# Kernel optimization log

Measured on AMD Instinct MI355X. Metric: run time of the kernel, lower is better.

The kernel has to match this reference:

```python
import jax, jax.numpy as jnp
import numpy as np

E = 256   # embed_dim
H = 8     # num_heads
D = E // H  # head_dim = 32
L = 1024  # seq len (Q_len == K_len == V_len)


def setup_inputs() -> dict:
    key = jax.random.key(0)
    ks = jax.random.split(key, 10)
    f = lambda k, s: jax.random.normal(k, s, dtype=jnp.float32)
    return {
        "V": f(ks[0], (L, E)),
        "K": f(ks[1], (L, E)),
        "Q": f(ks[2], (L, E)),
        # genomic-style coordinates, strictly positive
        "position": jax.random.uniform(ks[3], (L,), dtype=jnp.float32) * 1e5,
        "Wq": f(ks[4], (E, E)) * 0.02,
        "Wk": f(ks[5], (E, E)) * 0.02,
        "Wv": f(ks[6], (E, E)) * 0.02,
        "Wr": f(ks[7], (E, 1)) * 0.02,   # K_relative_linear weight [out=E, in=1]
        "Wo": f(ks[8], (E, E)) * 0.02,
        "bo": jnp.zeros((E,), jnp.float32),
    }


def reference(V, K, Q, position, Wq, Wk, Wv, Wr, Wo, bo):
    Lq = Q.shape[0]
    # projections (nn.Linear: x @ W.T), split into heads -> (L, H, D)
    q = (Q @ Wq.T).reshape(Lq, H, D)
    k = (K @ Wk.T).reshape(Lq, H, D)
    v = (V @ Wv.T).reshape(Lq, H, D)

    # relative position scalar per (q, k) pair: log(|p_q - p_k| + 1)
    rel = jnp.log(jnp.abs(position[:, None] - position[None, :]) + 1.0)  # (L, L)

    # K_relative_linear maps scalar rel -> (H, D); the einsum
    # 'nqhd,nhqjd->nhqj' then factorizes exactly as:
    #   sum_d Q[q,h,d] * rel[q,j] * Wr[h,d] = (Q . Wr)[h,q] * rel[q,j]
    # so we avoid materializing the (H, L, L, D) tensor while computing
    # mathematically identical results.
    Wr_h = Wr[:, 0].reshape(H, D)                    # (H, D)
    coeff = jnp.einsum('qhd,hd->hq', q, Wr_h)        # (H, L)

    energy = jnp.einsum('qhd,khd->hqk', q, k)        # (H, L, L)
    energy = energy + coeff[:, :, None] * rel[None, :, :]

    attn = jax.nn.softmax(energy / np.float32(E) ** 0.5, axis=2)
    out = jnp.einsum('hqk,khd->qhd', attn, v).reshape(Lq, E)
    out = out @ Wo.T + bo
    return out
```

## Files before the change

### kernel.cpp

```cpp
#include <hip/hip_runtime.h>
#include <math.h>

#define EDIM 256
#define LDIM 1024
#define HDIM 8
#define DDIM 32

typedef __attribute__((ext_vector_type(8))) short short8;
typedef __attribute__((ext_vector_type(4))) float f32x4;
typedef __attribute__((ext_vector_type(4))) unsigned u32x4;

__device__ inline unsigned short bf16h(float x) {
    unsigned u = __float_as_uint(x);
    return (unsigned short)((u + 0x7fff + ((u >> 16) & 1)) >> 16);
}
__device__ inline float bf16tof(unsigned short h) {
    return __uint_as_float(((unsigned)h) << 16);
}
__device__ inline unsigned packsplit(float x) {
    unsigned u = __float_as_uint(x);
    float r = x - __uint_as_float(u & 0xffff0000u);
    return (u & 0xffff0000u) | (unsigned)bf16h(r);
}
__device__ inline unsigned packsplit_rne(float x) {
    unsigned short h = bf16h(x);
    float r = x - bf16tof(h);
    return ((unsigned)h << 16) | (unsigned)bf16h(r);
}

__global__ __launch_bounds__(256) void proj_kernel(
    const float* __restrict__ Q, const float* __restrict__ Km, const float* __restrict__ V,
    const float* __restrict__ Wq, const float* __restrict__ Wk, const float* __restrict__ Wv,
    const float* __restrict__ Wr,
    unsigned* __restrict__ qT, unsigned* __restrict__ kT, unsigned* __restrict__ vT,
    float* __restrict__ coeff)
{
    const int z = blockIdx.z;
    const float* __restrict__ X = (z == 0) ? Q : (z == 1) ? Km : V;
    const float* __restrict__ W = (z == 0) ? Wq : (z == 1) ? Wk : Wv;
    unsigned* __restrict__ dst  = (z == 0) ? qT : (z == 1) ? kT : vT;

    const int n0 = blockIdx.x * 32;
    const int o0 = blockIdx.y * 32;
    const int tid = threadIdx.x;
    const int wave = tid >> 6, lane = tid & 63;
    const int n = lane & 15, quad = lane >> 4;
    const int rh = wave & 1, oh = wave >> 1;

    const int s    = tid >> 7;
    const int r    = (tid >> 2) & 31;
    const int qd   = tid & 3;
    const int half = r >> 4;
    const int fl8  = ((r & 15) | (qd << 4)) * 8;

    __shared__ short Xhi[2][2][512], Xlo[2][2][512];
    __shared__ short Whi[2][2][512], Wlo[2][2][512];
    __shared__ float cpart[2][2][16];

    const float* xp = X + (n0 + r) * EDIM + s * 32 + qd * 8;
    const float* wp = W + (o0 + r) * EDIM + s * 32 + qd * 8;

    float4 xa0 = *(const float4*)xp, xa1 = *(const float4*)(xp + 4);
    float4 wa0 = *(const float4*)wp, wa1 = *(const float4*)(wp + 4);

    f32x4 acc = {0.f, 0.f, 0.f, 0.f};

    for (int kb = 0; kb < EDIM; kb += 64) {
        __syncthreads();
        {
            float xv[8] = {xa0.x,xa0.y,xa0.z,xa0.w, xa1.x,xa1.y,xa1.z,xa1.w};
            float wv[8] = {wa0.x,wa0.y,wa0.z,wa0.w, wa1.x,wa1.y,wa1.z,wa1.w};
            short8 xh, xl, wh, wl;
            #pragma unroll
            for (int j = 0; j < 8; ++j) {
                unsigned px = packsplit_rne(xv[j]);
                unsigned pw = packsplit_rne(wv[j]);
                xh[j] = (short)(px >> 16); xl[j] = (short)(px & 0xffffu);
                wh[j] = (short)(pw >> 16); wl[j] = (short)(pw & 0xffffu);
            }
            *(short8*)&Xhi[s][half][fl8] = xh;
            *(short8*)&Xlo[s][half][fl8] = xl;
            *(short8*)&Whi[s][half][fl8] = wh;
            *(short8*)&Wlo[s][half][fl8] = wl;
        }
        float4 xn0, xn1, wn0, wn1;
        if (kb + 64 < EDIM) {
            xn0 = *(const float4*)(xp + kb + 64); xn1 = *(const float4*)(xp + kb + 68);
            wn0 = *(const float4*)(wp + kb + 64); wn1 = *(const float4*)(wp + kb + 68);
        }
        __syncthreads();
        #pragma unroll
        for (int ss = 0; ss < 2; ++ss) {
            short8 ah = *(const short8*)&Xhi[ss][rh][lane*8];
            short8 al = *(const short8*)&Xlo[ss][rh][lane*8];
            short8 bh = *(const short8*)&Whi[ss][oh][lane*8];
            short8 bl = *(const short8*)&Wlo[ss][oh][lane*8];
            acc = __builtin_amdgcn_mfma_f32_16x16x32_bf16(al, bh, acc, 0, 0, 0);
            acc = __builtin_amdgcn_mfma_f32_16x16x32_bf16(ah, bl, acc, 0, 0, 0);
            acc = __builtin_amdgcn_mfma_f32_16x16x32_bf16(ah, bh, acc, 0, 0, 0);
        }
        xa0 = xn0; xa1 = xn1; wa0 = wn0; wa1 = wn1;
    }

    const int h  = o0 >> 5;
    const int og = oh * 16 + n;
    #pragma unroll
    for (int i = 0; i < 4; ++i) {
        const int row = rh * 16 + 4 * quad + i;
        dst[(h * LDIM + n0 + row) * DDIM + og] = packsplit_rne(acc[i]);
    }

    if (z == 0) {
        const float wr = Wr[o0 + og];
        #pragma unroll
        for (int i = 0; i < 4; ++i) {
            float c = acc[i] * wr;
            c += __shfl_xor(c, 1, 64);
            c += __shfl_xor(c, 2, 64);
            c += __shfl_xor(c, 4, 64);
            c += __shfl_xor(c, 8, 64);
            if (n == 0) cpart[rh][oh][4*quad + i] = c;
        }
        __syncthreads();
        if (tid < 32)
            coeff[h * LDIM + n0 + tid] = cpart[tid >> 4][0][tid & 15]
                                       + cpart[tid >> 4][1][tid & 15];
    }
}

__global__ __launch_bounds__(256, 4) void attn_kernel(
    const unsigned* __restrict__ qT, const unsigned* __restrict__ kT, const unsigned* __restrict__ vT,
    const float* __restrict__ coeff, const float* __restrict__ pos,
    float* __restrict__ Op, float* __restrict__ Mp, float* __restrict__ Lp, int nkt)
{
    const int h   = blockIdx.y;
    const int q0  = blockIdx.x * 64;
    const int p   = blockIdx.z;
    const int kt0 = p * nkt * 64;
    const int tid  = threadIdx.x;
    const int wave = tid >> 6;
    const int lane = tid & 63;
    const int n    = lane & 15;
    const int quad = lane >> 4;
    const int qs0  = wave * 16;

    __shared__ __align__(16) short khi[4*64*8];
    __shared__ __align__(16) short klo[4*64*8];
    __shared__ __align__(16) unsigned vs2[32][68];
    __shared__ __align__(16) unsigned pA[64][68];
    __shared__ float pk[64];

    short8 qhi, qlo;
    {
        const unsigned* qp = qT + (h*LDIM + q0 + qs0 + n) * DDIM + quad*8;
        u32x4 a0 = *(const u32x4*)qp;
        u32x4 a1 = *(const u32x4*)(qp + 4);
        #pragma unroll
        for (int j = 0; j < 4; ++j) {
            qhi[j]   = (short)(a0[j] >> 16);  qlo[j]   = (short)(a0[j] & 0xffffu);
            qhi[j+4] = (short)(a1[j] >> 16);  qlo[j+4] = (short)(a1[j] & 0xffffu);
        }
    }

    float pq[4], cq[4];
    #pragma unroll
    for (int i = 0; i < 4; ++i) {
        const int r = q0 + qs0 + 4*quad + i;
        pq[i] = pos[r];
        cq[i] = coeff[h*LDIM + r] * 0.0625f;
    }

    float m[4], l[4];
    #pragma unroll
    for (int i = 0; i < 4; ++i) { m[i] = -INFINITY; l[i] = 0.f; }

    f32x4 of0 = {0.f,0.f,0.f,0.f}, of1 = {0.f,0.f,0.f,0.f};

    const int cS = tid >> 2;
    const int dq = tid & 3;
    const int lane2 = (cS & 15) | (dq << 4);
    const int gS = cS >> 4;

    u32x4 k0c, k1c, v0c, v1c; float pkc = 0.f;
    {
        const unsigned* kp = kT + (h*LDIM + kt0 + cS) * DDIM + dq*8;
        k0c = *(const u32x4*)kp; k1c = *(const u32x4*)(kp + 4);
        const unsigned* vp = vT + (h*LDIM + kt0 + cS) * DDIM + dq*8;
        v0c = *(const u32x4*)vp; v1c = *(const u32x4*)(vp + 4);
        if (tid < 64) pkc = pos[kt0 + tid];
    }

    for (int t = 0; t < nkt; ++t) {
        __syncthreads();

        {
            short8 hi8, lo8;
            #pragma unroll
            for (int j = 0; j < 4; ++j) {
                hi8[j]   = (short)(k0c[j] >> 16);  lo8[j]   = (short)(k0c[j] & 0xffffu);
                hi8[j+4] = (short)(k1c[j] >> 16);  lo8[j+4] = (short)(k1c[j] & 0xffffu);
            }
            *((short8*)&khi[(gS*64 + lane2)*8]) = hi8;
            *((short8*)&klo[(gS*64 + lane2)*8]) = lo8;
            #pragma unroll
            for (int j = 0; j < 4; ++j) {
                vs2[dq*8 + j][cS]     = v0c[j];
                vs2[dq*8 + j + 4][cS] = v1c[j];
            }
            if (tid < 64) pk[tid] = pkc;
        }

        u32x4 k0n, k1n, v0n, v1n; float pkn = 0.f;
        if (t + 1 < nkt) {
            const int kt = kt0 + (t+1) * 64;
            const unsigned* kp = kT + (h*LDIM + kt + cS) * DDIM + dq*8;
            k0n = *(const u32x4*)kp; k1n = *(const u32x4*)(kp + 4);
            const unsigned* vp = vT + (h*LDIM + kt + cS) * DDIM + dq*8;
            v0n = *(const u32x4*)vp; v1n = *(const u32x4*)(vp + 4);
            if (tid < 64) pkn = pos[kt + tid];
        }
        __syncthreads();

        f32x4 Sf[4];
        #pragma unroll
        for (int t4 = 0; t4 < 4; ++t4) {
            short8 bhi = *((const short8*)&khi[(t4*64 + lane)*8]);
            short8 blo = *((const short8*)&klo[(t4*64 + lane)*8]);
            f32x4 acc = {0.f, 0.f, 0.f, 0.f};
            acc = __builtin_amdgcn_mfma_f32_16x16x32_bf16(qlo, bhi, acc, 0, 0, 0);
            acc = __builtin_amdgcn_mfma_f32_16x16x32_bf16(qhi, blo, acc, 0, 0, 0);
            acc = __builtin_amdgcn_mfma_f32_16x16x32_bf16(qhi, bhi, acc, 0, 0, 0);
            Sf[t4] = acc;
        }

        float ev[4][4];
        float rmax[4] = {-INFINITY, -INFINITY, -INFINITY, -INFINITY};
        #pragma unroll
        for (int t4 = 0; t4 < 4; ++t4) {
            const float pkt = pk[16*t4 + n];
            #pragma unroll
            for (int i = 0; i < 4; ++i) {
                float s = fmaf(Sf[t4][i], 0.0625f, cq[i] * __logf(fabsf(pq[i] - pkt) + 1.f));
                ev[t4][i] = s;
                rmax[i] = fmaxf(rmax[i], s);
            }
        }
        #pragma unroll
        for (int off = 1; off < 16; off <<= 1)
            #pragma unroll
            for (int i = 0; i < 4; ++i)
                rmax[i] = fmaxf(rmax[i], __shfl_xor(rmax[i], off, 64));

        float al[4], rsum[4];
        #pragma unroll
        for (int i = 0; i < 4; ++i) {
            const float mn = fmaxf(m[i], rmax[i]);
            al[i] = __expf(m[i] - mn);
            m[i] = mn;
            rsum[i] = 0.f;
        }
        #pragma unroll
        for (int t4 = 0; t4 < 4; ++t4)
            #pragma unroll
            for (int i = 0; i < 4; ++i) {
                float e = __expf(ev[t4][i] - m[i]);
                rsum[i] += e;
                pA[qs0 + 4*quad + i][16*t4 + n] = packsplit(e);
            }
        #pragma unroll
        for (int off = 1; off < 16; off <<= 1)
            #pragma unroll
            for (int i = 0; i < 4; ++i)
                rsum[i] += __shfl_xor(rsum[i], off, 64);
        #pragma unroll
        for (int i = 0; i < 4; ++i) l[i] = l[i]*al[i] + rsum[i];

        #pragma unroll
        for (int i = 0; i < 4; ++i) { of0[i] *= al[i]; of1[i] *= al[i]; }

        #pragma unroll
        for (int ch = 0; ch < 2; ++ch) {
            const unsigned* ap = &pA[qs0 + n][ch*32 + quad*8];
            u32x4 a0 = *(const u32x4*)ap;
            u32x4 a1 = *(const u32x4*)(ap + 4);
            short8 phi, plo;
            #pragma unroll
            for (int j = 0; j < 4; ++j) {
                phi[j]   = (short)(a0[j] >> 16);
                plo[j]   = (short)(a0[j] & 0xffffu);
                phi[j+4] = (short)(a1[j] >> 16);
                plo[j+4] = (short)(a1[j] & 0xffffu);
            }
            #pragma unroll
            for (int dt = 0; dt < 2; ++dt) {
                const unsigned* vp = &vs2[dt*16 + n][ch*32 + quad*8];
                u32x4 b0 = *(const u32x4*)vp;
                u32x4 b1 = *(const u32x4*)(vp + 4);
                short8 vhi, vlo;
                #pragma unroll
                for (int j = 0; j < 4; ++j) {
                    vhi[j]   = (short)(b0[j] >> 16);
                    vlo[j]   = (short)(b0[j] & 0xffffu);
                    vhi[j+4] = (short)(b1[j] >> 16);
                    vlo[j+4] = (short)(b1[j] & 0xffffu);
                }
                f32x4& of = dt ? of1 : of0;
                of = __builtin_amdgcn_mfma_f32_16x16x32_bf16(plo, vhi, of, 0, 0, 0);
                of = __builtin_amdgcn_mfma_f32_16x16x32_bf16(phi, vlo, of, 0, 0, 0);
                of = __builtin_amdgcn_mfma_f32_16x16x32_bf16(phi, vhi, of, 0, 0, 0);
            }
        }

        k0c = k0n; k1c = k1n; v0c = v0n; v1c = v1n; pkc = pkn;
    }

    const int ph = p * HDIM + h;
    {
        const size_t base = ((size_t)ph * LDIM + q0 + qs0) * DDIM;
        #pragma unroll
        for (int i = 0; i < 4; ++i) {
            Op[base + (size_t)(4*quad + i)*DDIM + n]      = of0[i];
            Op[base + (size_t)(4*quad + i)*DDIM + 16 + n] = of1[i];
        }
    }
    if (n == 0) {
        #pragma unroll
        for (int i = 0; i < 4; ++i) {
            const int r = q0 + qs0 + 4*quad + i;
            Mp[ph*LDIM + r] = m[i];
            Lp[ph*LDIM + r] = l[i];
        }
    }
}

__global__ __launch_bounds__(256) void combine_kernel(
    const float* __restrict__ Op, const float* __restrict__ Mp, const float* __restrict__ Lp,
    int P, float* __restrict__ A)
{
    const int idx = blockIdx.x * 256 + threadIdx.x;
    const int n  = idx >> 6;
    const int e4 = (idx & 63) * 4;
    const int h  = e4 >> 5;
    const int d  = e4 & 31;

    float mv[8], lv[8];
    float mx = -INFINITY;
    #pragma unroll
    for (int p = 0; p < 8; ++p) if (p < P) {
        mv[p] = Mp[(p*HDIM + h)*LDIM + n];
        lv[p] = Lp[(p*HDIM + h)*LDIM + n];
        mx = fmaxf(mx, mv[p]);
    }
    float s = 0.f;
    #pragma unroll
    for (int p = 0; p < 8; ++p) if (p < P) {
        float a = __expf(mv[p] - mx);
        mv[p] = a;
        s += a * lv[p];
    }
    const float inv = 1.f / s;

    float4 x; x.x = x.y = x.z = x.w = 0.f;
    #pragma unroll
    for (int p = 0; p < 8; ++p) if (p < P) {
        const float sp = mv[p] * inv;
        float4 xp = *(const float4*)(Op + ((size_t)(p*HDIM + h)*LDIM + n)*DDIM + d);
        x.x += sp*xp.x; x.y += sp*xp.y; x.z += sp*xp.z; x.w += sp*xp.w;
    }
    *(float4*)(A + n*EDIM + e4) = x;
}

__global__ __launch_bounds__(256) void outproj_kernel(
    const float* __restrict__ A, const float* __restrict__ Wo,
    const float* __restrict__ bo, float* __restrict__ out)
{
    const int n0 = blockIdx.x * 32;
    const int o0 = blockIdx.y * 32;
    const int tid = threadIdx.x;
    const int wave = tid >> 6, lane = tid & 63;
    const int n = lane & 15, quad = lane >> 4;
    const int rh = wave & 1, oh = wave >> 1;

    const int s    = tid >> 7;
    const int r    = (tid >> 2) & 31;
    const int qd   = tid & 3;
    const int half = r >> 4;
    const int fl8  = ((r & 15) | (qd << 4)) * 8;

    __shared__ short Xhi[2][2][512], Xlo[2][2][512];
    __shared__ short Whi[2][2][512], Wlo[2][2][512];

    const float* xp = A  + (n0 + r) * EDIM + s * 32 + qd * 8;
    const float* wp = Wo + (o0 + r) * EDIM + s * 32 + qd * 8;

    float4 xa0 = *(const float4*)xp, xa1 = *(const float4*)(xp + 4);
    float4 wa0 = *(const float4*)wp, wa1 = *(const float4*)(wp + 4);

    f32x4 acc = {0.f, 0.f, 0.f, 0.f};

    for (int kb = 0; kb < EDIM; kb += 64) {
        __syncthreads();
        {
            float xv[8] = {xa0.x,xa0.y,xa0.z,xa0.w, xa1.x,xa1.y,xa1.z,xa1.w};
            float wv[8] = {wa0.x,wa0.y,wa0.z,wa0.w, wa1.x,wa1.y,wa1.z,wa1.w};
            short8 xh, xl, wh, wl;
            #pragma unroll
            for (int j = 0; j < 8; ++j) {
                unsigned px = packsplit_rne(xv[j]);
                unsigned pw = packsplit_rne(wv[j]);
                xh[j] = (short)(px >> 16); xl[j] = (short)(px & 0xffffu);
                wh[j] = (short)(pw >> 16); wl[j] = (short)(pw & 0xffffu);
            }
            *(short8*)&Xhi[s][half][fl8] = xh;
            *(short8*)&Xlo[s][half][fl8] = xl;
            *(short8*)&Whi[s][half][fl8] = wh;
            *(short8*)&Wlo[s][half][fl8] = wl;
        }
        float4 xn0, xn1, wn0, wn1;
        if (kb + 64 < EDIM) {
            xn0 = *(const float4*)(xp + kb + 64); xn1 = *(const float4*)(xp + kb + 68);
            wn0 = *(const float4*)(wp + kb + 64); wn1 = *(const float4*)(wp + kb + 68);
        }
        __syncthreads();
        #pragma unroll
        for (int ss = 0; ss < 2; ++ss) {
            short8 ah = *(const short8*)&Xhi[ss][rh][lane*8];
            short8 al = *(const short8*)&Xlo[ss][rh][lane*8];
            short8 bh = *(const short8*)&Whi[ss][oh][lane*8];
            short8 bl = *(const short8*)&Wlo[ss][oh][lane*8];
            acc = __builtin_amdgcn_mfma_f32_16x16x32_bf16(al, bh, acc, 0, 0, 0);
            acc = __builtin_amdgcn_mfma_f32_16x16x32_bf16(ah, bl, acc, 0, 0, 0);
            acc = __builtin_amdgcn_mfma_f32_16x16x32_bf16(ah, bh, acc, 0, 0, 0);
        }
        xa0 = xn0; xa1 = xn1; wa0 = wn0; wa1 = wn1;
    }

    const int og = o0 + oh*16 + n;
    const float b = bo[og];
    #pragma unroll
    for (int i = 0; i < 4; ++i) {
        const int row = n0 + rh*16 + 4*quad + i;
        out[row * EDIM + og] = acc[i] + b;
    }
}

extern "C" void kernel_launch(void* const* d_in, const int* in_sizes, int n_in,
                              void* d_out, int out_size, void* d_ws, size_t ws_size,
                              hipStream_t stream) {
    const float* V   = (const float*)d_in[0];
    const float* K   = (const float*)d_in[1];
    const float* Q   = (const float*)d_in[2];
    const float* pos = (const float*)d_in[3];
    const float* Wq  = (const float*)d_in[4];
    const float* Wk  = (const float*)d_in[5];
    const float* Wv  = (const float*)d_in[6];
    const float* Wr  = (const float*)d_in[7];
    const float* Wo  = (const float*)d_in[8];
    const float* bo  = (const float*)d_in[9];
    float* out = (float*)d_out;
    float* ws  = (float*)d_ws;

    auto need = [](int P) -> size_t {
        return (size_t)(794624 + P*278528) * 4;
    };
    int P = 2;
    if (ws_size >= need(8)) P = 8;
    else if (ws_size >= need(4)) P = 4;

    unsigned* qT = (unsigned*)ws;
    unsigned* kT = (unsigned*)(ws + 262144);
    unsigned* vT = (unsigned*)(ws + 524288);
    float* coeff = ws + 786432;
    float* Op    = ws + 794624;
    float* Mp    = Op + (size_t)P * 262144;
    float* Lp    = Mp + (size_t)P * 8192;
    float* A     = ws;

    proj_kernel   <<<dim3(32, 8, 3), 256, 0, stream>>>(Q, K, V, Wq, Wk, Wv, Wr, qT, kT, vT, coeff);
    attn_kernel   <<<dim3(16, 8, P), 256, 0, stream>>>(qT, kT, vT, coeff, pos, Op, Mp, Lp, 16 / P);
    combine_kernel<<<dim3(256),      256, 0, stream>>>(Op, Mp, Lp, P, A);
    outproj_kernel<<<dim3(32, 8),    256, 0, stream>>>(A, Wo, bo, out);
}
```

Baseline: 106.8 us.

## Store bf16 hi/lo planes separately, fuse combine with out-projection, use exp2/log2

Projection outputs are now written as separate bf16 hi and lo arrays, so the attention kernel loads MFMA operands directly without unpacking. The same planar layout is used for the P tile and the V tile in shared memory. Exp and log switch to the hardware exp2/log2 instructions, with the softmax scale folded into a log2e-adjusted constant. The combine and output-projection kernels are merged into one kernel that reads a pre-split Wo produced by an extra z-slice of the projection launch, removing one launch and the intermediate A buffer. The fused final kernel runs only 128 blocks and leaves half of its MFMA rows unused, so it may expose less parallelism than the old pair of kernels.

```diff
diff --git a/kernel.cpp b/kernel.cpp
--- a/kernel.cpp
+++ b/kernel.cpp
@@ -8,7 +8,6 @@
 
 typedef __attribute__((ext_vector_type(8))) short short8;
 typedef __attribute__((ext_vector_type(4))) float f32x4;
-typedef __attribute__((ext_vector_type(4))) unsigned u32x4;
 
 __device__ inline unsigned short bf16h(float x) {
     unsigned u = __float_as_uint(x);
@@ -17,32 +16,43 @@
 __device__ inline float bf16tof(unsigned short h) {
     return __uint_as_float(((unsigned)h) << 16);
 }
-__device__ inline unsigned packsplit(float x) {
-    unsigned u = __float_as_uint(x);
-    float r = x - __uint_as_float(u & 0xffff0000u);
-    return (u & 0xffff0000u) | (unsigned)bf16h(r);
-}
-__device__ inline unsigned packsplit_rne(float x) {
-    unsigned short h = bf16h(x);
-    float r = x - bf16tof(h);
-    return ((unsigned)h << 16) | (unsigned)bf16h(r);
-}
+__device__ inline float exp2fast(float x) {
+    float r; asm volatile("v_exp_f32 %0, %1" : "=v"(r) : "v"(x)); return r;
+}
+__device__ inline float log2fast(float x) {
+    float r; asm volatile("v_log_f32 %0, %1" : "=v"(r) : "v"(x)); return r;
+}
+
+#define SC2 0.09016843880556021f
 
 __global__ __launch_bounds__(256) void proj_kernel(
     const float* __restrict__ Q, const float* __restrict__ Km, const float* __restrict__ V,
     const float* __restrict__ Wq, const float* __restrict__ Wk, const float* __restrict__ Wv,
-    const float* __restrict__ Wr,
-    unsigned* __restrict__ qT, unsigned* __restrict__ kT, unsigned* __restrict__ vT,
-    float* __restrict__ coeff)
+    const float* __restrict__ Wr, const float* __restrict__ Wo,
+    short* __restrict__ qThi, short* __restrict__ qTlo,
+    short* __restrict__ kThi, short* __restrict__ kTlo,
+    short* __restrict__ vThi, short* __restrict__ vTlo,
+    float* __restrict__ coeff, short* __restrict__ Wohi, short* __restrict__ Wolo)
 {
     const int z = blockIdx.z;
+    const int tid = threadIdx.x;
+
+    if (z == 3) {
+        const int idx = ((blockIdx.y * 32 + blockIdx.x) << 8) + tid;
+        const float w = Wo[idx];
+        const unsigned short hh = bf16h(w);
+        Wohi[idx] = (short)hh;
+        Wolo[idx] = (short)bf16h(w - bf16tof(hh));
+        return;
+    }
+
     const float* __restrict__ X = (z == 0) ? Q : (z == 1) ? Km : V;
     const float* __restrict__ W = (z == 0) ? Wq : (z == 1) ? Wk : Wv;
-    unsigned* __restrict__ dst  = (z == 0) ? qT : (z == 1) ? kT : vT;
+    short* __restrict__ dhi     = (z == 0) ? qThi : (z == 1) ? kThi : vThi;
+    short* __restrict__ dlo     = (z == 0) ? qTlo : (z == 1) ? kTlo : vTlo;
 
     const int n0 = blockIdx.x * 32;
     const int o0 = blockIdx.y * 32;
-    const int tid = threadIdx.x;
     const int wave = tid >> 6, lane = tid & 63;
     const int n = lane & 15, quad = lane >> 4;
     const int rh = wave & 1, oh = wave >> 1;
@@ -73,10 +83,10 @@
             short8 xh, xl, wh, wl;
             #pragma unroll
             for (int j = 0; j < 8; ++j) {
-                unsigned px = packsplit_rne(xv[j]);
-                unsigned pw = packsplit_rne(wv[j]);
-                xh[j] = (short)(px >> 16); xl[j] = (short)(px & 0xffffu);
-                wh[j] = (short)(pw >> 16); wl[j] = (short)(pw & 0xffffu);
+                unsigned short xhh = bf16h(xv[j]);
+                unsigned short whh = bf16h(wv[j]);
+                xh[j] = (short)xhh; xl[j] = (short)bf16h(xv[j] - bf16tof(xhh));
+                wh[j] = (short)whh; wl[j] = (short)bf16h(wv[j] - bf16tof(whh));
             }
             *(short8*)&Xhi[s][half][fl8] = xh;
             *(short8*)&Xlo[s][half][fl8] = xl;
@@ -107,7 +117,9 @@
     #pragma unroll
     for (int i = 0; i < 4; ++i) {
         const int row = rh * 16 + 4 * quad + i;
-        dst[(h * LDIM + n0 + row) * DDIM + og] = packsplit_rne(acc[i]);
+        const unsigned short hh = bf16h(acc[i]);
+        dhi[(h * LDIM + n0 + row) * DDIM + og] = (short)hh;
+        dlo[(h * LDIM + n0 + row) * DDIM + og] = (short)bf16h(acc[i] - bf16tof(hh));
     }
 
     if (z == 0) {
@@ -129,7 +141,9 @@
 }
 
 __global__ __launch_bounds__(256, 4) void attn_kernel(
-    const unsigned* __restrict__ qT, const unsigned* __restrict__ kT, const unsigned* __restrict__ vT,
+    const short* __restrict__ qThi, const short* __restrict__ qTlo,
+    const short* __restrict__ kThi, const short* __restrict__ kTlo,
+    const short* __restrict__ vThi, const short* __restrict__ vTlo,
     const float* __restrict__ coeff, const float* __restrict__ pos,
     float* __restrict__ Op, float* __restrict__ Mp, float* __restrict__ Lp, int nkt)
 {
@@ -146,21 +160,14 @@
 
     __shared__ __align__(16) short khi[4*64*8];
     __shared__ __align__(16) short klo[4*64*8];
-    __shared__ __align__(16) unsigned vs2[32][68];
-    __shared__ __align__(16) unsigned pA[64][68];
+    __shared__ __align__(16) short vs_hi[32][72];
+    __shared__ __align__(16) short vs_lo[32][72];
+    __shared__ __align__(16) short pa_hi[64][72];
+    __shared__ __align__(16) short pa_lo[64][72];
     __shared__ float pk[64];
 
-    short8 qhi, qlo;
-    {
-        const unsigned* qp = qT + (h*LDIM + q0 + qs0 + n) * DDIM + quad*8;
-        u32x4 a0 = *(const u32x4*)qp;
-        u32x4 a1 = *(const u32x4*)(qp + 4);
-        #pragma unroll
-        for (int j = 0; j < 4; ++j) {
-            qhi[j]   = (short)(a0[j] >> 16);  qlo[j]   = (short)(a0[j] & 0xffffu);
-            qhi[j+4] = (short)(a1[j] >> 16);  qlo[j+4] = (short)(a1[j] & 0xffffu);
-        }
-    }
+    const short8 qhi = *(const short8*)(qThi + (h*LDIM + q0 + qs0 + n) * DDIM + quad*8);
+    const short8 qlo = *(const short8*)(qTlo + (h*LDIM + q0 + qs0 + n) * DDIM + quad*8);
 
     float pq[4], cq[4];
     #pragma unroll
@@ -181,43 +188,36 @@
     const int lane2 = (cS & 15) | (dq << 4);
     const int gS = cS >> 4;
 
-    u32x4 k0c, k1c, v0c, v1c; float pkc = 0.f;
+    short8 khi_c, klo_c, vhi_c, vlo_c; float pkc = 0.f;
     {
-        const unsigned* kp = kT + (h*LDIM + kt0 + cS) * DDIM + dq*8;
-        k0c = *(const u32x4*)kp; k1c = *(const u32x4*)(kp + 4);
-        const unsigned* vp = vT + (h*LDIM + kt0 + cS) * DDIM + dq*8;
-        v0c = *(const u32x4*)vp; v1c = *(const u32x4*)(vp + 4);
+        const int off = (h*LDIM + kt0 + cS) * DDIM + dq*8;
+        khi_c = *(const short8*)(kThi + off);
+        klo_c = *(const short8*)(kTlo + off);
+        vhi_c = *(const short8*)(vThi + off);
+        vlo_c = *(const short8*)(vTlo + off);
         if (tid < 64) pkc = pos[kt0 + tid];
     }
 
     for (int t = 0; t < nkt; ++t) {
         __syncthreads();
 
-        {
-            short8 hi8, lo8;
-            #pragma unroll
-            for (int j = 0; j < 4; ++j) {
-                hi8[j]   = (short)(k0c[j] >> 16);  lo8[j]   = (short)(k0c[j] & 0xffffu);
-                hi8[j+4] = (short)(k1c[j] >> 16);  lo8[j+4] = (short)(k1c[j] & 0xffffu);
-            }
-            *((short8*)&khi[(gS*64 + lane2)*8]) = hi8;
-            *((short8*)&klo[(gS*64 + lane2)*8]) = lo8;
-            #pragma unroll
-            for (int j = 0; j < 4; ++j) {
-                vs2[dq*8 + j][cS]     = v0c[j];
-                vs2[dq*8 + j + 4][cS] = v1c[j];
-            }
-            if (tid < 64) pk[tid] = pkc;
-        }
-
-        u32x4 k0n, k1n, v0n, v1n; float pkn = 0.f;
+        *((short8*)&khi[(gS*64 + lane2)*8]) = khi_c;
+        *((short8*)&klo[(gS*64 + lane2)*8]) = klo_c;
+        #pragma unroll
+        for (int j = 0; j < 8; ++j) {
+            vs_hi[dq*8 + j][cS] = vhi_c[j];
+            vs_lo[dq*8 + j][cS] = vlo_c[j];
+        }
+        if (tid < 64) pk[tid] = pkc;
+
+        short8 khi_n, klo_n, vhi_n, vlo_n; float pkn = 0.f;
         if (t + 1 < nkt) {
-            const int kt = kt0 + (t+1) * 64;
-            const unsigned* kp = kT + (h*LDIM + kt + cS) * DDIM + dq*8;
-            k0n = *(const u32x4*)kp; k1n = *(const u32x4*)(kp + 4);
-            const unsigned* vp = vT + (h*LDIM + kt + cS) * DDIM + dq*8;
-            v0n = *(const u32x4*)vp; v1n = *(const u32x4*)(vp + 4);
-            if (tid < 64) pkn = pos[kt + tid];
+            const int off = (h*LDIM + kt0 + (t+1)*64 + cS) * DDIM + dq*8;
+            khi_n = *(const short8*)(kThi + off);
+            klo_n = *(const short8*)(kTlo + off);
+            vhi_n = *(const short8*)(vThi + off);
+            vlo_n = *(const short8*)(vTlo + off);
+            if (tid < 64) pkn = pos[kt0 + (t+1)*64 + tid];
         }
         __syncthreads();
 
@@ -240,7 +240,7 @@
             const float pkt = pk[16*t4 + n];
             #pragma unroll
             for (int i = 0; i < 4; ++i) {
-                float s = fmaf(Sf[t4][i], 0.0625f, cq[i] * __logf(fabsf(pq[i] - pkt) + 1.f));
+                float s = fmaf(Sf[t4][i], SC2, cq[i] * log2fast(fabsf(pq[i] - pkt) + 1.f));
                 ev[t4][i] = s;
                 rmax[i] = fmaxf(rmax[i], s);
             }
@@ -255,7 +255,7 @@
         #pragma unroll
         for (int i = 0; i < 4; ++i) {
             const float mn = fmaxf(m[i], rmax[i]);
-            al[i] = __expf(m[i] - mn);
+            al[i] = exp2fast(m[i] - mn);
             m[i] = mn;
             rsum[i] = 0.f;
         }
@@ -263,9 +263,12 @@
         for (int t4 = 0; t4 < 4; ++t4)
             #pragma unroll
             for (int i = 0; i < 4; ++i) {
-                float e = __expf(ev[t4][i] - m[i]);
+                float e = exp2fast(ev[t4][i] - m[i]);
                 rsum[i] += e;
-                pA[qs0 + 4*quad + i][16*t4 + n] = packsplit(e);
+                unsigned u = __float_as_uint(e);
+                pa_hi[qs0 + 4*quad + i][16*t4 + n] = (short)(u >> 16);
+                float r = e - __uint_as_float(u & 0xffff0000u);
+                pa_lo[qs0 + 4*quad + i][16*t4 + n] = (short)bf16h(r);
             }
         #pragma unroll
         for (int off = 1; off < 16; off <<= 1)
@@ -280,38 +283,20 @@
 
         #pragma unroll
         for (int ch = 0; ch < 2; ++ch) {
-            const unsigned* ap = &pA[qs0 + n][ch*32 + quad*8];
-            u32x4 a0 = *(const u32x4*)ap;
-            u32x4 a1 = *(const u32x4*)(ap + 4);
-            short8 phi, plo;
-            #pragma unroll
-            for (int j = 0; j < 4; ++j) {
-                phi[j]   = (short)(a0[j] >> 16);
-                plo[j]   = (short)(a0[j] & 0xffffu);
-                phi[j+4] = (short)(a1[j] >> 16);
-                plo[j+4] = (short)(a1[j] & 0xffffu);
+            short8 phi = *(const short8*)&pa_hi[qs0 + n][ch*32 + quad*8];
+            short8 plo = *(const short8*)&pa_lo[qs0 + n][ch*32 + quad*8];
+            #pragma unroll
+            for (int dt = 0; dt < 2; ++dt) {
+                short8 vh8 = *(const short8*)&vs_hi[dt*16 + n][ch*32 + quad*8];
+                short8 vl8 = *(const short8*)&vs_lo[dt*16 + n][ch*32 + quad*8];
+                f32x4& of = dt ? of1 : of0;
+                of = __builtin_amdgcn_mfma_f32_16x16x32_bf16(plo, vh8, of, 0, 0, 0);
+                of = __builtin_amdgcn_mfma_f32_16x16x32_bf16(phi, vl8, of, 0, 0, 0);
+                of = __builtin_amdgcn_mfma_f32_16x16x32_bf16(phi, vh8, of, 0, 0, 0);
             }
-            #pragma unroll
-            for (int dt = 0; dt < 2; ++dt) {
-                const unsigned* vp = &vs2[dt*16 + n][ch*32 + quad*8];
-                u32x4 b0 = *(const u32x4*)vp;
-                u32x4 b1 = *(const u32x4*)(vp + 4);
-                short8 vhi, vlo;
-                #pragma unroll
-                for (int j = 0; j < 4; ++j) {
-                    vhi[j]   = (short)(b0[j] >> 16);
-                    vlo[j]   = (short)(b0[j] & 0xffffu);
-                    vhi[j+4] = (short)(b1[j] >> 16);
-                    vlo[j+4] = (short)(b1[j] & 0xffffu);
-                }
-                f32x4& of = dt ? of1 : of0;
-                of = __builtin_amdgcn_mfma_f32_16x16x32_bf16(plo, vhi, of, 0, 0, 0);
-                of = __builtin_amdgcn_mfma_f32_16x16x32_bf16(phi, vlo, of, 0, 0, 0);
-                of = __builtin_amdgcn_mfma_f32_16x16x32_bf16(phi, vhi, of, 0, 0, 0);
-            }
-        }
-
-        k0c = k0n; k1c = k1n; v0c = v0n; v1c = v1n; pkc = pkn;
+        }
+
+        khi_c = khi_n; klo_c = klo_n; vhi_c = vhi_n; vlo_c = vlo_n; pkc = pkn;
     }
 
     const int ph = p * HDIM + h;
@@ -333,114 +318,94 @@
     }
 }
 
-__global__ __launch_bounds__(256) void combine_kernel(
+__global__ __launch_bounds__(256) void finale_kernel(
     const float* __restrict__ Op, const float* __restrict__ Mp, const float* __restrict__ Lp,
-    int P, float* __restrict__ A)
+    const short* __restrict__ Wohi, const short* __restrict__ Wolo,
+    const float* __restrict__ bo, int P, float* __restrict__ out)
 {
-    const int idx = blockIdx.x * 256 + threadIdx.x;
-    const int n  = idx >> 6;
-    const int e4 = (idx & 63) * 4;
-    const int h  = e4 >> 5;
-    const int d  = e4 & 31;
-
-    float mv[8], lv[8];
-    float mx = -INFINITY;
-    #pragma unroll
-    for (int p = 0; p < 8; ++p) if (p < P) {
-        mv[p] = Mp[(p*HDIM + h)*LDIM + n];
-        lv[p] = Lp[(p*HDIM + h)*LDIM + n];
-        mx = fmaxf(mx, mv[p]);
-    }
-    float s = 0.f;
-    #pragma unroll
-    for (int p = 0; p < 8; ++p) if (p < P) {
-        float a = __expf(mv[p] - mx);
-        mv[p] = a;
-        s += a * lv[p];
-    }
-    const float inv = 1.f / s;
-
-    float4 x; x.x = x.y = x.z = x.w = 0.f;
-    #pragma unroll
-    for (int p = 0; p < 8; ++p) if (p < P) {
-        const float sp = mv[p] * inv;
-        float4 xp = *(const float4*)(Op + ((size_t)(p*HDIM + h)*LDIM + n)*DDIM + d);
-        x.x += sp*xp.x; x.y += sp*xp.y; x.z += sp*xp.z; x.w += sp*xp.w;
-    }
-    *(float4*)(A + n*EDIM + e4) = x;
-}
-
-__global__ __launch_bounds__(256) void outproj_kernel(
-    const float* __restrict__ A, const float* __restrict__ Wo,
-    const float* __restrict__ bo, float* __restrict__ out)
-{
-    const int n0 = blockIdx.x * 32;
-    const int o0 = blockIdx.y * 32;
+    const int n0 = blockIdx.x * 8;
     const int tid = threadIdx.x;
+
+    __shared__ __align__(16) short Ahi[8][264], Alo[8][264];
+
+    {
+        const int r  = tid >> 5;
+        const int c8 = (tid & 31) * 8;
+        const int hh = c8 >> 5;
+        const int d  = c8 & 31;
+        float mv[8], lv[8];
+        float mx = -INFINITY;
+        #pragma unroll
+        for (int p = 0; p < 8; ++p) if (p < P) {
+            mv[p] = Mp[(p*HDIM + hh)*LDIM + n0 + r];
+            lv[p] = Lp[(p*HDIM + hh)*LDIM + n0 + r];
+            mx = fmaxf(mx, mv[p]);
+        }
+        float s = 0.f;
+        #pragma unroll
+        for (int p = 0; p < 8; ++p) if (p < P) {
+            float a = exp2fast(mv[p] - mx);
+            mv[p] = a;
+            s += a * lv[p];
+        }
+        const float inv = 1.f / s;
+        float a[8] = {0.f,0.f,0.f,0.f,0.f,0.f,0.f,0.f};
+        #pragma unroll
+        for (int p = 0; p < 8; ++p) if (p < P) {
+            const float sp = mv[p] * inv;
+            const float* op = Op + ((size_t)(p*HDIM + hh)*LDIM + n0 + r)*DDIM + d;
+            float4 x0 = *(const float4*)op;
+            float4 x1 = *(const float4*)(op + 4);
+            a[0] += sp*x0.x; a[1] += sp*x0.y; a[2] += sp*x0.z; a[3] += sp*x0.w;
+            a[4] += sp*x1.x; a[5] += sp*x1.y; a[6] += sp*x1.z; a[7] += sp*x1.w;
+        }
+        short8 ah8, al8;
+        #pragma unroll
+        for (int j = 0; j < 8; ++j) {
+            const unsigned short hhh = bf16h(a[j]);
+            ah8[j] = (short)hhh;
+            al8[j] = (short)bf16h(a[j] - bf16tof(hhh));
+        }
+        *(short8*)&Ahi[r][c8] = ah8;
+        *(short8*)&Alo[r][c8] = al8;
+    }
+    __syncthreads();
+
     const int wave = tid >> 6, lane = tid & 63;
     const int n = lane & 15, quad = lane >> 4;
-    const int rh = wave & 1, oh = wave >> 1;
-
-    const int s    = tid >> 7;
-    const int r    = (tid >> 2) & 31;
-    const int qd   = tid & 3;
-    const int half = r >> 4;
-    const int fl8  = ((r & 15) | (qd << 4)) * 8;
-
-    __shared__ short Xhi[2][2][512], Xlo[2][2][512];
-    __shared__ short Whi[2][2][512], Wlo[2][2][512];
-
-    const float* xp = A  + (n0 + r) * EDIM + s * 32 + qd * 8;
-    const float* wp = Wo + (o0 + r) * EDIM + s * 32 + qd * 8;
-
-    float4 xa0 = *(const float4*)xp, xa1 = *(const float4*)(xp + 4);
-    float4 wa0 = *(const float4*)wp, wa1 = *(const float4*)(wp + 4);
-
-    f32x4 acc = {0.f, 0.f, 0.f, 0.f};
-
-    for (int kb = 0; kb < EDIM; kb += 64) {
-        __syncthreads();
-        {
-            float xv[8] = {xa0.x,xa0.y,xa0.z,xa0.w, xa1.x,xa1.y,xa1.z,xa1.w};
-            float wv[8] = {wa0.x,wa0.y,wa0.z,wa0.w, wa1.x,wa1.y,wa1.z,wa1.w};
-            short8 xh, xl, wh, wl;
-            #pragma unroll
-            for (int j = 0; j < 8; ++j) {
-                unsigned px = packsplit_rne(xv[j]);
-                unsigned pw = packsplit_rne(wv[j]);
-                xh[j] = (short)(px >> 16); xl[j] = (short)(px & 0xffffu);
-                wh[j] = (short)(pw >> 16); wl[j] = (short)(pw & 0xffffu);
+    const int ow = wave * 64;
+    const int rA = n & 7;
+
+    f32x4 acc[4];
+    #pragma unroll
+    for (int cf = 0; cf < 4; ++cf) { acc[cf][0]=0.f; acc[cf][1]=0.f; acc[cf][2]=0.f; acc[cf][3]=0.f; }
+
+    #pragma unroll
+    for (int kk = 0; kk < 8; ++kk) {
+        short8 ah = *(const short8*)&Ahi[rA][kk*32 + quad*8];
+        short8 al = *(const short8*)&Alo[rA][kk*32 + quad*8];
+        #pragma unroll
+        for (int cf = 0; cf < 4; ++cf) {
+            const int o = ow + cf*16 + n;
+            short8 bh = *(const short8*)(Wohi + o*EDIM + kk*32 + quad*8);
+            short8 bl = *(const short8*)(Wolo + o*EDIM + kk*32 + quad*8);
+            acc[cf] = __builtin_amdgcn_mfma_f32_16x16x32_bf16(al, bh, acc[cf], 0, 0, 0);
+            acc[cf] = __builtin_amdgcn_mfma_f32_16x16x32_bf16(ah, bl, acc[cf], 0, 0, 0);
+            acc[cf] = __builtin_amdgcn_mfma_f32_16x16x32_bf16(ah, bh, acc[cf], 0, 0, 0);
+        }
+    }
+
+    if (quad < 2) {
+        #pragma unroll
+        for (int cf = 0; cf < 4; ++cf) {
+            const int o = ow + cf*16 + n;
+            const float b = bo[o];
+            #pragma unroll
+            for (int i = 0; i < 4; ++i) {
+                const int row = n0 + 4*quad + i;
+                out[row*EDIM + o] = acc[cf][i] + b;
             }
-            *(short8*)&Xhi[s][half][fl8] = xh;
-            *(short8*)&Xlo[s][half][fl8] = xl;
-            *(short8*)&Whi[s][half][fl8] = wh;
-            *(short8*)&Wlo[s][half][fl8] = wl;
-        }
-        float4 xn0, xn1, wn0, wn1;
-        if (kb + 64 < EDIM) {
-            xn0 = *(const float4*)(xp + kb + 64); xn1 = *(const float4*)(xp + kb + 68);
-            wn0 = *(const float4*)(wp + kb + 64); wn1 = *(const float4*)(wp + kb + 68);
-        }
-        __syncthreads();
-        #pragma unroll
-        for (int ss = 0; ss < 2; ++ss) {
-            short8 ah = *(const short8*)&Xhi[ss][rh][lane*8];
-            short8 al = *(const short8*)&Xlo[ss][rh][lane*8];
-            short8 bh = *(const short8*)&Whi[ss][oh][lane*8];
-            short8 bl = *(const short8*)&Wlo[ss][oh][lane*8];
-            acc = __builtin_amdgcn_mfma_f32_16x16x32_bf16(al, bh, acc, 0, 0, 0);
-            acc = __builtin_amdgcn_mfma_f32_16x16x32_bf16(ah, bl, acc, 0, 0, 0);
-            acc = __builtin_amdgcn_mfma_f32_16x16x32_bf16(ah, bh, acc, 0, 0, 0);
-        }
-        xa0 = xn0; xa1 = xn1; wa0 = wn0; wa1 = wn1;
-    }
-
-    const int og = o0 + oh*16 + n;
-    const float b = bo[og];
-    #pragma unroll
-    for (int i = 0; i < 4; ++i) {
-        const int row = n0 + rh*16 + 4*quad + i;
-        out[row * EDIM + og] = acc[i] + b;
+        }
     }
 }
 
@@ -458,26 +423,30 @@
     const float* Wo  = (const float*)d_in[8];
     const float* bo  = (const float*)d_in[9];
     float* out = (float*)d_out;
-    float* ws  = (float*)d_ws;
-
-    auto need = [](int P) -> size_t {
-        return (size_t)(794624 + P*278528) * 4;
-    };
+    char* base = (char*)d_ws;
+
+    auto need = [](int P) -> size_t { return 3440640 + (size_t)P * 1114112; };
     int P = 2;
     if (ws_size >= need(8)) P = 8;
     else if (ws_size >= need(4)) P = 4;
 
-    unsigned* qT = (unsigned*)ws;
-    unsigned* kT = (unsigned*)(ws + 262144);
-    unsigned* vT = (unsigned*)(ws + 524288);
-    float* coeff = ws + 786432;
-    float* Op    = ws + 794624;
+    short* qThi  = (short*)(base);
+    short* qTlo  = (short*)(base + 524288);
+    short* kThi  = (short*)(base + 1048576);
+    short* kTlo  = (short*)(base + 1572864);
+    short* vThi  = (short*)(base + 2097152);
+    short* vTlo  = (short*)(base + 2621440);
+    float* coeff = (float*)(base + 3145728);
+    short* Wohi  = (short*)(base + 3178496);
+    short* Wolo  = (short*)(base + 3309568);
+    float* Op    = (float*)(base + 3440640);
     float* Mp    = Op + (size_t)P * 262144;
     float* Lp    = Mp + (size_t)P * 8192;
-    float* A     = ws;
-
-    proj_kernel   <<<dim3(32, 8, 3), 256, 0, stream>>>(Q, K, V, Wq, Wk, Wv, Wr, qT, kT, vT, coeff);
-    attn_kernel   <<<dim3(16, 8, P), 256, 0, stream>>>(qT, kT, vT, coeff, pos, Op, Mp, Lp, 16 / P);
-    combine_kernel<<<dim3(256),      256, 0, stream>>>(Op, Mp, Lp, P, A);
-    outproj_kernel<<<dim3(32, 8),    256, 0, stream>>>(A, Wo, bo, out);
-}
+
+    proj_kernel  <<<dim3(32, 8, 4), 256, 0, stream>>>(Q, K, V, Wq, Wk, Wv, Wr, Wo,
+                                                      qThi, qTlo, kThi, kTlo, vThi, vTlo,
+                                                      coeff, Wohi, Wolo);
+    attn_kernel  <<<dim3(16, 8, P), 256, 0, stream>>>(qThi, qTlo, kThi, kTlo, vThi, vTlo,
+                                                      coeff, pos, Op, Mp, Lp, 16 / P);
+    finale_kernel<<<dim3(128),      256, 0, stream>>>(Op, Mp, Lp, Wohi, Wolo, bo, P, out);
+}
```

Measured after the change: 109.8 us. +2.9%, slower.
